# Performance work log

Measured on AMD Instinct MI355X. Metric: run time of the kernel, lower is better.

## Reference

```python
import jax, jax.numpy as jnp
import numpy as np

C = 64
C2 = C // 2

def setup_inputs() -> dict:
    key = jax.random.key(0)
    ks = jax.random.split(key, 5)
    x = jax.random.normal(ks[0], (8, C, 64, 64), dtype=jnp.float32)
    # 1x1 conv weights stored as [out, in] matrices (kernel size 1)
    g_w = jax.random.normal(ks[1], (C2, C), dtype=jnp.float32) * (1.0 / np.sqrt(C))
    g_b = jax.random.normal(ks[2], (C2,), dtype=jnp.float32) * 0.01
    W_w = jax.random.normal(ks[3], (C, C2), dtype=jnp.float32) * (1.0 / np.sqrt(C2))
    W_b = jax.random.normal(ks[4], (C,), dtype=jnp.float32) * 0.01
    return {"x": x, "g_w": g_w, "g_b": g_b, "W_w": W_w, "W_b": W_b}

def reference(x, g_w, g_b, W_w, W_b):
    b, c, h, w = x.shape
    xf = x.reshape(b, c, h * w)                      # [B, C, N]
    # g: 1x1 conv -> [B, N, C2]
    g_x = jnp.einsum('oc,bcn->bno', g_w, xf) + g_b
    # attention scores on raw x (theta/phi convs unused in original forward)
    f = jnp.einsum('bcn,bcm->bnm', xf, xf)           # [B, N, N]
    f_div_C = jax.nn.softmax(f, axis=-1)
    y = jnp.einsum('bnm,bmo->bno', f_div_C, g_x)     # [B, N, C2]
    # W: 1x1 conv back to C channels, then residual
    W_y = jnp.einsum('co,bno->bcn', W_w, y) + W_b[None, :, None]
    z = W_y.reshape(b, c, h, w) + x
    return z
```

## Files before the change

kernel.cpp:

```cpp
#include <hip/hip_runtime.h>
#include <hip/hip_bf16.h>

#define BATCH 8
#define CH    64
#define CH2   32
#define NN    4096
#define BN    (BATCH * NN)
#define YPAD  36
#define RPAD  40
#define MAXSPLIT 8

typedef __attribute__((ext_vector_type(8)))  short        short8;
typedef __attribute__((ext_vector_type(4)))  float        floatx4;
typedef __attribute__((ext_vector_type(16))) float        floatx16;
typedef __attribute__((ext_vector_type(4)))  unsigned int uint4v;
typedef __attribute__((ext_vector_type(8)))  unsigned short ushort8v;
typedef unsigned short ushort_t;

#define LOG2E      1.4426950408889634f
#define SQRT_LOG2E 1.2011224087864498f

__device__ __forceinline__ unsigned short f2bf_rne(float f) {
    unsigned int u = __float_as_uint(f);
    return (unsigned short)((u + 0x7FFFu + ((u >> 16) & 1u)) >> 16);
}


__global__ __launch_bounds__(256) void prep_fused(const float* __restrict__ x,
                                                  const float* __restrict__ gw,
                                                  const float* __restrict__ gb,
                                                  ushort_t* __restrict__ xF,
                                                  float* __restrict__ mlog,
                                                  ushort_t* __restrict__ gxF) {
    __shared__ float gwl[CH2 * CH];
    __shared__ float gbl[CH2];
    int t = threadIdx.x;
    for (int i = t; i < CH2 * CH; i += 256) gwl[i] = gw[i];
    if (t < CH2) gbl[t] = gb[t];
    __syncthreads();

    int g   = blockIdx.x * 256 + t;
    int row = g >> 2;
    int q4  = g & 3;
    int b = row >> 12, n = row & (NN - 1);
    const float* xp = x + (size_t)b * CH * NN + n;

    float xv[16];
    #pragma unroll
    for (int j = 0; j < 16; ++j) xv[j] = xp[(size_t)(q4 * 16 + j) * NN];

    float ns = 0.f;
    short8 v0, v1;
    #pragma unroll
    for (int j = 0; j < 8; ++j) {
        ns += xv[j] * xv[j];
        v0[j] = (short)f2bf_rne(xv[j] * SQRT_LOG2E);
    }
    #pragma unroll
    for (int j = 0; j < 8; ++j) {
        ns += xv[8 + j] * xv[8 + j];
        v1[j] = (short)f2bf_rne(xv[8 + j] * SQRT_LOG2E);
    }
    {
        size_t pb8 = (((size_t)b * 128 + (n >> 5)) * 4 + q4) * 2;
        *(short8*)(xF + pb8 * 256 + (size_t)(n & 31) * 8)       = v0;
        *(short8*)(xF + (pb8 + 1) * 256 + (size_t)(n & 31) * 8) = v1;
    }
    ns += __shfl_xor(ns, 1);
    ns += __shfl_xor(ns, 2);
    if (q4 == 0) mlog[row] = 12.0f * sqrtf(ns) * LOG2E;

    float acc[CH2];
    #pragma unroll
    for (int o = 0; o < CH2; ++o) {
        const float4* wr = (const float4*)(gwl + o * CH + q4 * 16);
        float4 w0 = wr[0], w1 = wr[1], w2 = wr[2], w3 = wr[3];
        float a;
        a  = w0.x * xv[0]  + w0.y * xv[1]  + w0.z * xv[2]  + w0.w * xv[3];
        a += w1.x * xv[4]  + w1.y * xv[5]  + w1.z * xv[6]  + w1.w * xv[7];
        a += w2.x * xv[8]  + w2.y * xv[9]  + w2.z * xv[10] + w2.w * xv[11];
        a += w3.x * xv[12] + w3.y * xv[13] + w3.z * xv[14] + w3.w * xv[15];
        acc[o] = a;
    }
    #pragma unroll
    for (int o = 0; o < CH2; ++o) {
        acc[o] += __shfl_xor(acc[o], 1);
        acc[o] += __shfl_xor(acc[o], 2);
    }
    {
        size_t vbase = (((size_t)b * 256 + (n >> 4)) * 2 + ((n >> 3) & 1)) * 256 + (n & 7);
        #pragma unroll
        for (int i = 0; i < 8; ++i) {
            int o = q4 * 8 + i;
            gxF[vbase + (size_t)o * 8] = f2bf_rne(acc[o] + gbl[o]);
        }
    }
}

__global__ __launch_bounds__(256, 4) void flash_attn(const ushort_t* __restrict__ xF,
                                                     const ushort_t* __restrict__ gxF,
                                                     const float* __restrict__ mlog,
                                                     ushort_t* __restrict__ py,
                                                     float* __restrict__ pl,
                                                     int ksplit) {
    __shared__ __align__(16) unsigned char smem[18432];

    const int tid = threadIdx.x, wave = tid >> 6, lane = tid & 63;
    const int q5 = lane & 31;
    const int h  = lane >> 5;
    const int bq = blockIdx.x & 255;
    const int sp = blockIdx.x >> 8;
    const int b = bq >> 5, qt = bq & 31;
    const int n0 = qt * 128 + wave * 32;
    const int k0 = sp * ksplit;

    short8 qf[4];
    {
        const ushort_t* qp = xF + ((((size_t)b * 128 + qt * 4 + wave) * 4) * 2 + h) * 256 + q5 * 8;
        #pragma unroll
        for (int f = 0; f < 4; ++f) qf[f] = *(const short8*)(qp + f * 512);
    }
    const float ml = mlog[(size_t)b * NN + n0 + q5];

    floatx16 yt;
    #pragma unroll
    for (int i = 0; i < 16; ++i) yt[i] = 0.f;
    float ls0 = 0.f, ls1 = 0.f;

    const int nsub = ksplit >> 5;
    const ushort_t* kp = xF + ((((size_t)b * 128 + (k0 >> 5)) * 4) * 2 + h) * 256 + q5 * 8;
    const ushort_t* vp = gxF + (((size_t)b * 256 + (k0 >> 4)) * 2 + h) * 256 + q5 * 8;

    for (int s = 0; s < nsub; ++s) {
        const ushort_t* kps = kp + (size_t)s * 2048;
        short8 kf0 = *(const short8*)(kps);
        short8 kf1 = *(const short8*)(kps + 512);
        short8 kf2 = *(const short8*)(kps + 1024);
        short8 kf3 = *(const short8*)(kps + 1536);
        short8 vf0 = *(const short8*)(vp + (size_t)(s * 2) * 512);
        short8 vf1 = *(const short8*)(vp + (size_t)(s * 2 + 1) * 512);

        floatx16 st;
        #pragma unroll
        for (int i = 0; i < 16; ++i) st[i] = 0.f;
        st = __builtin_amdgcn_mfma_f32_32x32x16_bf16(kf0, qf[0], st, 0, 0, 0);
        st = __builtin_amdgcn_mfma_f32_32x32x16_bf16(kf1, qf[1], st, 0, 0, 0);
        st = __builtin_amdgcn_mfma_f32_32x32x16_bf16(kf2, qf[2], st, 0, 0, 0);
        st = __builtin_amdgcn_mfma_f32_32x32x16_bf16(kf3, qf[3], st, 0, 0, 0);

        #pragma unroll
        for (int fp = 0; fp < 2; ++fp) {
            unsigned int d0, d1, d2, d3;
            {
                float p0 = __builtin_amdgcn_exp2f(st[fp * 8 + 0] - ml);
                float p1 = __builtin_amdgcn_exp2f(st[fp * 8 + 1] - ml);
                float p2 = __builtin_amdgcn_exp2f(st[fp * 8 + 2] - ml);
                float p3 = __builtin_amdgcn_exp2f(st[fp * 8 + 3] - ml);
                float p4 = __builtin_amdgcn_exp2f(st[fp * 8 + 4] - ml);
                float p5 = __builtin_amdgcn_exp2f(st[fp * 8 + 5] - ml);
                float p6 = __builtin_amdgcn_exp2f(st[fp * 8 + 6] - ml);
                float p7 = __builtin_amdgcn_exp2f(st[fp * 8 + 7] - ml);
                ls0 += p0 + p2;
                ls1 += p1 + p3;
                ls0 += p4 + p6;
                ls1 += p5 + p7;
                asm("v_cvt_pk_bf16_f32 %0, %1, %2" : "=v"(d0) : "v"(p0), "v"(p1));
                asm("v_cvt_pk_bf16_f32 %0, %1, %2" : "=v"(d1) : "v"(p2), "v"(p3));
                asm("v_cvt_pk_bf16_f32 %0, %1, %2" : "=v"(d2) : "v"(p4), "v"(p5));
                asm("v_cvt_pk_bf16_f32 %0, %1, %2" : "=v"(d3) : "v"(p6), "v"(p7));
            }
            asm("v_permlane32_swap_b32 %0, %1" : "+v"(d0), "+v"(d2));
            asm("v_permlane32_swap_b32 %0, %1" : "+v"(d1), "+v"(d3));
            uint4v bv;
            bv[0] = d0; bv[1] = d1; bv[2] = d2; bv[3] = d3;
            short8 pb = __builtin_bit_cast(short8, bv);
            short8 vf = fp ? vf1 : vf0;
            yt = __builtin_amdgcn_mfma_f32_32x32x16_bf16(vf, pb, yt, 0, 0, 0);
        }
    }

    float lsum = ls0 + ls1;
    lsum += __shfl_xor(lsum, 32);

    float* yb = (float*)smem + wave * 32 * YPAD;
    #pragma unroll
    for (int reg = 0; reg < 16; ++reg) {
        int o = (reg & 3) + 8 * (reg >> 2) + 4 * h;
        yb[q5 * YPAD + o] = yt[reg];
    }
    __syncthreads();
    {
        int qq = lane >> 1, half = lane & 1;
        const float* src = yb + qq * YPAD + half * 16;
        float4 s0 = *(const float4*)(src);
        float4 s1 = *(const float4*)(src + 4);
        float4 s2 = *(const float4*)(src + 8);
        float4 s3 = *(const float4*)(src + 12);
        ushort8v pk0, pk1;
        pk0[0] = f2bf_rne(s0.x); pk0[1] = f2bf_rne(s0.y);
        pk0[2] = f2bf_rne(s0.z); pk0[3] = f2bf_rne(s0.w);
        pk0[4] = f2bf_rne(s1.x); pk0[5] = f2bf_rne(s1.y);
        pk0[6] = f2bf_rne(s1.z); pk0[7] = f2bf_rne(s1.w);
        pk1[0] = f2bf_rne(s2.x); pk1[1] = f2bf_rne(s2.y);
        pk1[2] = f2bf_rne(s2.z); pk1[3] = f2bf_rne(s2.w);
        pk1[4] = f2bf_rne(s3.x); pk1[5] = f2bf_rne(s3.y);
        pk1[6] = f2bf_rne(s3.z); pk1[7] = f2bf_rne(s3.w);
        ushort_t* dst = py + ((size_t)sp * BN + (size_t)b * NN + n0 + qq) * CH2 + half * 16;
        *(ushort8v*)(dst)     = pk0;
        *(ushort8v*)(dst + 8) = pk1;
    }
    if (h == 0) pl[(size_t)sp * BN + (size_t)b * NN + n0 + q5] = lsum;
}

__global__ __launch_bounds__(256) void reduce_proj(const ushort_t* __restrict__ py,
                                                   const float* __restrict__ pl,
                                                   const float* __restrict__ Ww,
                                                   const float* __restrict__ Wb,
                                                   const float* __restrict__ x,
                                                   float* __restrict__ out,
                                                   int nsplit) {
    __shared__ ushort_t WwB[CH * RPAD];
    __shared__ ushort_t Y[64 * RPAD];
    __shared__ float    linv[64];
    __shared__ float    WbL[CH];

    const int t = threadIdx.x;
    const int row = t >> 2, o8 = (t & 3) * 8;
    const int grow0 = blockIdx.x * 64;

    {
        const float* wp = Ww + row * CH2 + o8;
        ushort8v w;
        #pragma unroll
        for (int j = 0; j < 8; ++j) w[j] = f2bf_rne(wp[j]);
        *(ushort8v*)(&WwB[row * RPAD + o8]) = w;
    }
    if (t < CH) WbL[t] = Wb[t];
    if (t < 64) {
        const float* plp = pl + grow0 + t;
        float lv[MAXSPLIT];
        #pragma unroll
        for (int s = 0; s < MAXSPLIT; ++s) {
            int sc = s < nsplit ? s : 0;
            lv[s] = plp[(size_t)sc * BN];
        }
        float l = 0.f;
        #pragma unroll
        for (int s = 0; s < MAXSPLIT; ++s) if (s < nsplit) l += lv[s];
        linv[t] = 1.0f / l;
    }

    float acc[8];
    #pragma unroll
    for (int j = 0; j < 8; ++j) acc[j] = 0.f;
    {
        const ushort_t* pp = py + ((size_t)(grow0 + row)) * CH2 + o8;
        ushort8v pv[MAXSPLIT];
        #pragma unroll
        for (int s = 0; s < MAXSPLIT; ++s) {
            int sc = s < nsplit ? s : 0;
            pv[s] = *(const ushort8v*)(pp + (size_t)sc * BN * CH2);
        }
        #pragma unroll
        for (int s = 0; s < MAXSPLIT; ++s) if (s < nsplit) {
            #pragma unroll
            for (int j = 0; j < 8; ++j)
                acc[j] += __uint_as_float((unsigned int)pv[s][j] << 16);
        }
    }
    __syncthreads();
    {
        float inv = linv[row];
        ushort8v yv;
        #pragma unroll
        for (int j = 0; j < 8; ++j) yv[j] = f2bf_rne(acc[j] * inv);
        *(ushort8v*)(&Y[row * RPAD + o8]) = yv;
    }
    __syncthreads();

    const int wave = t >> 6, lane = t & 63;
    const int ql = lane & 15, quad = lane >> 4;
    const int b = grow0 >> 12;
    const int nbase = (grow0 & (NN - 1)) + wave * 16;

    short8 bfrag = *(const short8*)(&Y[(wave * 16 + ql) * RPAD + quad * 8]);
    #pragma unroll
    for (int ct = 0; ct < 4; ++ct) {
        short8 afrag = *(const short8*)(&WwB[(ct * 16 + ql) * RPAD + quad * 8]);
        floatx4 d = (floatx4){0.f, 0.f, 0.f, 0.f};
        d = __builtin_amdgcn_mfma_f32_16x16x32_bf16(afrag, bfrag, d, 0, 0, 0);
        #pragma unroll
        for (int r = 0; r < 4; ++r) {
            int c = ct * 16 + quad * 4 + r;
            size_t oi = ((size_t)b * CH + c) * NN + nbase + ql;
            out[oi] = d[r] + WbL[c] + x[oi];
        }
    }
}

extern "C" void kernel_launch(void* const* d_in, const int* in_sizes, int n_in,
                              void* d_out, int out_size, void* d_ws, size_t ws_size,
                              hipStream_t stream) {
    const float* x  = (const float*)d_in[0];
    const float* gw = (const float*)d_in[1];
    const float* gb = (const float*)d_in[2];
    const float* Ww = (const float*)d_in[3];
    const float* Wb = (const float*)d_in[4];
    float* out = (float*)d_out;

    ushort_t* xF   = (ushort_t*)d_ws;
    ushort_t* gxF  = xF + (size_t)BN * CH;
    float*    mlog = (float*)(gxF + (size_t)BATCH * CH2 * NN);
    ushort_t* py   = (ushort_t*)(mlog + BN);
    size_t base_bytes = (size_t)BN * CH * 2 + (size_t)BATCH * CH2 * NN * 2 + (size_t)BN * 4;
    int split = MAXSPLIT;
    while (split > 1 && base_bytes + (size_t)split * BN * (CH2 * 2 + 4) > ws_size)
        split >>= 1;
    float* pl = (float*)(py + (size_t)split * BN * CH2);

    hipLaunchKernelGGL(prep_fused,  dim3(BN * 4 / 256), dim3(256), 0, stream,
                       x, gw, gb, xF, mlog, gxF);
    hipLaunchKernelGGL(flash_attn,  dim3(256 * split),  dim3(256), 0, stream,
                       xF, gxF, mlog, py, pl, NN / split);
    hipLaunchKernelGGL(reduce_proj, dim3(BN / 64),      dim3(256), 0, stream,
                       py, pl, Ww, Wb, x, out, split);
}
```

Before: 118.8 us.

## Process two query tiles per wave to reuse K/V fragment loads

Each wave now handles 64 query rows as two 32-row tiles, A and B. Every K and V fragment loaded from global memory feeds MFMAs for both tiles, which halves K/V load traffic per query and interleaves the two independent MFMA chains for better latency hiding. The grid shrinks from 256 to 128 blocks per split, the occupancy hint in launch_bounds is dropped, and the main loop is kept rolled. The cost is roughly double the register use for accumulators and Q fragments, lower occupancy, and fewer blocks in flight.

```diff
diff --git a/kernel.cpp b/kernel.cpp
--- a/kernel.cpp
+++ b/kernel.cpp
@@ -97,73 +97,83 @@
     }
 }
 
-__global__ __launch_bounds__(256, 4) void flash_attn(const ushort_t* __restrict__ xF,
-                                                     const ushort_t* __restrict__ gxF,
-                                                     const float* __restrict__ mlog,
-                                                     ushort_t* __restrict__ py,
-                                                     float* __restrict__ pl,
-                                                     int ksplit) {
+__global__ __launch_bounds__(256) void flash_attn(const ushort_t* __restrict__ xF,
+                                                  const ushort_t* __restrict__ gxF,
+                                                  const float* __restrict__ mlog,
+                                                  ushort_t* __restrict__ py,
+                                                  float* __restrict__ pl,
+                                                  int ksplit) {
     __shared__ __align__(16) unsigned char smem[18432];
 
     const int tid = threadIdx.x, wave = tid >> 6, lane = tid & 63;
     const int q5 = lane & 31;
     const int h  = lane >> 5;
-    const int bq = blockIdx.x & 255;
-    const int sp = blockIdx.x >> 8;
-    const int b = bq >> 5, qt = bq & 31;
-    const int n0 = qt * 128 + wave * 32;
+    const int bq = blockIdx.x & 127;
+    const int sp = blockIdx.x >> 7;
+    const int b = bq >> 4, qseg = bq & 15;
+    const int n0A = qseg * 256 + wave * 64;
+    const int n0B = n0A + 32;
     const int k0 = sp * ksplit;
 
-    short8 qf[4];
-    {
-        const ushort_t* qp = xF + ((((size_t)b * 128 + qt * 4 + wave) * 4) * 2 + h) * 256 + q5 * 8;
-        #pragma unroll
-        for (int f = 0; f < 4; ++f) qf[f] = *(const short8*)(qp + f * 512);
-    }
-    const float ml = mlog[(size_t)b * NN + n0 + q5];
-
-    floatx16 yt;
-    #pragma unroll
-    for (int i = 0; i < 16; ++i) yt[i] = 0.f;
-    float ls0 = 0.f, ls1 = 0.f;
+    short8 qfA[4], qfB[4];
+    {
+        const ushort_t* qpA = xF + ((((size_t)b * 128 + (n0A >> 5)) * 4) * 2 + h) * 256 + q5 * 8;
+        #pragma unroll
+        for (int f = 0; f < 4; ++f) {
+            qfA[f] = *(const short8*)(qpA + f * 512);
+            qfB[f] = *(const short8*)(qpA + 2048 + f * 512);
+        }
+    }
+    const float mlA = mlog[(size_t)b * NN + n0A + q5];
+    const float mlB = mlog[(size_t)b * NN + n0B + q5];
+
+    floatx16 zc;
+    #pragma unroll
+    for (int i = 0; i < 16; ++i) zc[i] = 0.f;
+
+    floatx16 ytA, ytB;
+    #pragma unroll
+    for (int i = 0; i < 16; ++i) { ytA[i] = 0.f; ytB[i] = 0.f; }
+    float lsA = 0.f, lsB = 0.f;
 
     const int nsub = ksplit >> 5;
     const ushort_t* kp = xF + ((((size_t)b * 128 + (k0 >> 5)) * 4) * 2 + h) * 256 + q5 * 8;
     const ushort_t* vp = gxF + (((size_t)b * 256 + (k0 >> 4)) * 2 + h) * 256 + q5 * 8;
 
+    #pragma unroll 1
     for (int s = 0; s < nsub; ++s) {
         const ushort_t* kps = kp + (size_t)s * 2048;
         short8 kf0 = *(const short8*)(kps);
         short8 kf1 = *(const short8*)(kps + 512);
         short8 kf2 = *(const short8*)(kps + 1024);
         short8 kf3 = *(const short8*)(kps + 1536);
-        short8 vf0 = *(const short8*)(vp + (size_t)(s * 2) * 512);
-        short8 vf1 = *(const short8*)(vp + (size_t)(s * 2 + 1) * 512);
-
-        floatx16 st;
-        #pragma unroll
-        for (int i = 0; i < 16; ++i) st[i] = 0.f;
-        st = __builtin_amdgcn_mfma_f32_32x32x16_bf16(kf0, qf[0], st, 0, 0, 0);
-        st = __builtin_amdgcn_mfma_f32_32x32x16_bf16(kf1, qf[1], st, 0, 0, 0);
-        st = __builtin_amdgcn_mfma_f32_32x32x16_bf16(kf2, qf[2], st, 0, 0, 0);
-        st = __builtin_amdgcn_mfma_f32_32x32x16_bf16(kf3, qf[3], st, 0, 0, 0);
+        short8 vf0 = *(const short8*)(vp + (size_t)s * 1024);
+        short8 vf1 = *(const short8*)(vp + (size_t)s * 1024 + 512);
+
+        floatx16 stA, stB;
+        stA = __builtin_amdgcn_mfma_f32_32x32x16_bf16(kf0, qfA[0], zc,  0, 0, 0);
+        stB = __builtin_amdgcn_mfma_f32_32x32x16_bf16(kf0, qfB[0], zc,  0, 0, 0);
+        stA = __builtin_amdgcn_mfma_f32_32x32x16_bf16(kf1, qfA[1], stA, 0, 0, 0);
+        stB = __builtin_amdgcn_mfma_f32_32x32x16_bf16(kf1, qfB[1], stB, 0, 0, 0);
+        stA = __builtin_amdgcn_mfma_f32_32x32x16_bf16(kf2, qfA[2], stA, 0, 0, 0);
+        stB = __builtin_amdgcn_mfma_f32_32x32x16_bf16(kf2, qfB[2], stB, 0, 0, 0);
+        stA = __builtin_amdgcn_mfma_f32_32x32x16_bf16(kf3, qfA[3], stA, 0, 0, 0);
+        stB = __builtin_amdgcn_mfma_f32_32x32x16_bf16(kf3, qfB[3], stB, 0, 0, 0);
 
         #pragma unroll
         for (int fp = 0; fp < 2; ++fp) {
             unsigned int d0, d1, d2, d3;
             {
-                float p0 = __builtin_amdgcn_exp2f(st[fp * 8 + 0] - ml);
-                float p1 = __builtin_amdgcn_exp2f(st[fp * 8 + 1] - ml);
-                float p2 = __builtin_amdgcn_exp2f(st[fp * 8 + 2] - ml);
-                float p3 = __builtin_amdgcn_exp2f(st[fp * 8 + 3] - ml);
-                float p4 = __builtin_amdgcn_exp2f(st[fp * 8 + 4] - ml);
-                float p5 = __builtin_amdgcn_exp2f(st[fp * 8 + 5] - ml);
-                float p6 = __builtin_amdgcn_exp2f(st[fp * 8 + 6] - ml);
-                float p7 = __builtin_amdgcn_exp2f(st[fp * 8 + 7] - ml);
-                ls0 += p0 + p2;
-                ls1 += p1 + p3;
-                ls0 += p4 + p6;
-                ls1 += p5 + p7;
+                float p0 = __builtin_amdgcn_exp2f(stA[fp * 8 + 0] - mlA);
+                float p1 = __builtin_amdgcn_exp2f(stA[fp * 8 + 1] - mlA);
+                float p2 = __builtin_amdgcn_exp2f(stA[fp * 8 + 2] - mlA);
+                float p3 = __builtin_amdgcn_exp2f(stA[fp * 8 + 3] - mlA);
+                float p4 = __builtin_amdgcn_exp2f(stA[fp * 8 + 4] - mlA);
+                float p5 = __builtin_amdgcn_exp2f(stA[fp * 8 + 5] - mlA);
+                float p6 = __builtin_amdgcn_exp2f(stA[fp * 8 + 6] - mlA);
+                float p7 = __builtin_amdgcn_exp2f(stA[fp * 8 + 7] - mlA);
+                lsA += (p0 + p2) + (p4 + p6);
+                lsA += (p1 + p3) + (p5 + p7);
                 asm("v_cvt_pk_bf16_f32 %0, %1, %2" : "=v"(d0) : "v"(p0), "v"(p1));
                 asm("v_cvt_pk_bf16_f32 %0, %1, %2" : "=v"(d1) : "v"(p2), "v"(p3));
                 asm("v_cvt_pk_bf16_f32 %0, %1, %2" : "=v"(d2) : "v"(p4), "v"(p5));
@@ -174,42 +184,72 @@
             uint4v bv;
             bv[0] = d0; bv[1] = d1; bv[2] = d2; bv[3] = d3;
             short8 pb = __builtin_bit_cast(short8, bv);
-            short8 vf = fp ? vf1 : vf0;
-            yt = __builtin_amdgcn_mfma_f32_32x32x16_bf16(vf, pb, yt, 0, 0, 0);
-        }
-    }
-
-    float lsum = ls0 + ls1;
-    lsum += __shfl_xor(lsum, 32);
+            ytA = __builtin_amdgcn_mfma_f32_32x32x16_bf16(fp ? vf1 : vf0, pb, ytA, 0, 0, 0);
+        }
+        #pragma unroll
+        for (int fp = 0; fp < 2; ++fp) {
+            unsigned int d0, d1, d2, d3;
+            {
+                float p0 = __builtin_amdgcn_exp2f(stB[fp * 8 + 0] - mlB);
+                float p1 = __builtin_amdgcn_exp2f(stB[fp * 8 + 1] - mlB);
+                float p2 = __builtin_amdgcn_exp2f(stB[fp * 8 + 2] - mlB);
+                float p3 = __builtin_amdgcn_exp2f(stB[fp * 8 + 3] - mlB);
+                float p4 = __builtin_amdgcn_exp2f(stB[fp * 8 + 4] - mlB);
+                float p5 = __builtin_amdgcn_exp2f(stB[fp * 8 + 5] - mlB);
+                float p6 = __builtin_amdgcn_exp2f(stB[fp * 8 + 6] - mlB);
+                float p7 = __builtin_amdgcn_exp2f(stB[fp * 8 + 7] - mlB);
+                lsB += (p0 + p2) + (p4 + p6);
+                lsB += (p1 + p3) + (p5 + p7);
+                asm("v_cvt_pk_bf16_f32 %0, %1, %2" : "=v"(d0) : "v"(p0), "v"(p1));
+                asm("v_cvt_pk_bf16_f32 %0, %1, %2" : "=v"(d1) : "v"(p2), "v"(p3));
+                asm("v_cvt_pk_bf16_f32 %0, %1, %2" : "=v"(d2) : "v"(p4), "v"(p5));
+                asm("v_cvt_pk_bf16_f32 %0, %1, %2" : "=v"(d3) : "v"(p6), "v"(p7));
+            }
+            asm("v_permlane32_swap_b32 %0, %1" : "+v"(d0), "+v"(d2));
+            asm("v_permlane32_swap_b32 %0, %1" : "+v"(d1), "+v"(d3));
+            uint4v bv;
+            bv[0] = d0; bv[1] = d1; bv[2] = d2; bv[3] = d3;
+            short8 pb = __builtin_bit_cast(short8, bv);
+            ytB = __builtin_amdgcn_mfma_f32_32x32x16_bf16(fp ? vf1 : vf0, pb, ytB, 0, 0, 0);
+        }
+    }
+
+    lsA += __shfl_xor(lsA, 32);
+    lsB += __shfl_xor(lsB, 32);
 
     float* yb = (float*)smem + wave * 32 * YPAD;
     #pragma unroll
-    for (int reg = 0; reg < 16; ++reg) {
-        int o = (reg & 3) + 8 * (reg >> 2) + 4 * h;
-        yb[q5 * YPAD + o] = yt[reg];
-    }
-    __syncthreads();
-    {
-        int qq = lane >> 1, half = lane & 1;
-        const float* src = yb + qq * YPAD + half * 16;
-        float4 s0 = *(const float4*)(src);
-        float4 s1 = *(const float4*)(src + 4);
-        float4 s2 = *(const float4*)(src + 8);
-        float4 s3 = *(const float4*)(src + 12);
-        ushort8v pk0, pk1;
-        pk0[0] = f2bf_rne(s0.x); pk0[1] = f2bf_rne(s0.y);
-        pk0[2] = f2bf_rne(s0.z); pk0[3] = f2bf_rne(s0.w);
-        pk0[4] = f2bf_rne(s1.x); pk0[5] = f2bf_rne(s1.y);
-        pk0[6] = f2bf_rne(s1.z); pk0[7] = f2bf_rne(s1.w);
-        pk1[0] = f2bf_rne(s2.x); pk1[1] = f2bf_rne(s2.y);
-        pk1[2] = f2bf_rne(s2.z); pk1[3] = f2bf_rne(s2.w);
-        pk1[4] = f2bf_rne(s3.x); pk1[5] = f2bf_rne(s3.y);
-        pk1[6] = f2bf_rne(s3.z); pk1[7] = f2bf_rne(s3.w);
-        ushort_t* dst = py + ((size_t)sp * BN + (size_t)b * NN + n0 + qq) * CH2 + half * 16;
-        *(ushort8v*)(dst)     = pk0;
-        *(ushort8v*)(dst + 8) = pk1;
-    }
-    if (h == 0) pl[(size_t)sp * BN + (size_t)b * NN + n0 + q5] = lsum;
+    for (int pass = 0; pass < 2; ++pass) {
+        const int n0 = pass ? n0B : n0A;
+        #pragma unroll
+        for (int reg = 0; reg < 16; ++reg) {
+            int o = (reg & 3) + 8 * (reg >> 2) + 4 * h;
+            yb[q5 * YPAD + o] = pass ? ytB[reg] : ytA[reg];
+        }
+        __syncthreads();
+        {
+            int qq = lane >> 1, half = lane & 1;
+            const float* src = yb + qq * YPAD + half * 16;
+            float4 s0 = *(const float4*)(src);
+            float4 s1 = *(const float4*)(src + 4);
+            float4 s2 = *(const float4*)(src + 8);
+            float4 s3 = *(const float4*)(src + 12);
+            ushort8v pk0, pk1;
+            pk0[0] = f2bf_rne(s0.x); pk0[1] = f2bf_rne(s0.y);
+            pk0[2] = f2bf_rne(s0.z); pk0[3] = f2bf_rne(s0.w);
+            pk0[4] = f2bf_rne(s1.x); pk0[5] = f2bf_rne(s1.y);
+            pk0[6] = f2bf_rne(s1.z); pk0[7] = f2bf_rne(s1.w);
+            pk1[0] = f2bf_rne(s2.x); pk1[1] = f2bf_rne(s2.y);
+            pk1[2] = f2bf_rne(s2.z); pk1[3] = f2bf_rne(s2.w);
+            pk1[4] = f2bf_rne(s3.x); pk1[5] = f2bf_rne(s3.y);
+            pk1[6] = f2bf_rne(s3.z); pk1[7] = f2bf_rne(s3.w);
+            ushort_t* dst = py + ((size_t)sp * BN + (size_t)b * NN + n0 + qq) * CH2 + half * 16;
+            *(ushort8v*)(dst)     = pk0;
+            *(ushort8v*)(dst + 8) = pk1;
+        }
+        __syncthreads();
+        if (h == 0) pl[(size_t)sp * BN + (size_t)b * NN + n0 + q5] = pass ? lsB : lsA;
+    }
 }
 
 __global__ __launch_bounds__(256) void reduce_proj(const ushort_t* __restrict__ py,
@@ -320,7 +360,7 @@
 
     hipLaunchKernelGGL(prep_fused,  dim3(BN * 4 / 256), dim3(256), 0, stream,
                        x, gw, gb, xF, mlog, gxF);
-    hipLaunchKernelGGL(flash_attn,  dim3(256 * split),  dim3(256), 0, stream,
+    hipLaunchKernelGGL(flash_attn,  dim3(128 * split),  dim3(256), 0, stream,
                        xF, gxF, mlog, py, pl, NN / split);
     hipLaunchKernelGGL(reduce_proj, dim3(BN / 64),      dim3(256), 0, stream,
                        py, pl, Ww, Wb, x, out, split);
```

After: 121.7 us. +2.4%, slower.
